# Kernel optimization log

Hardware: AMD Instinct MI355X
Metric: run time of the kernel (lower is better)

## Reference

```python
import jax, jax.numpy as jnp
import numpy as np

B, T, C_IN, H, W = 4, 3, 64, 64, 64
E = 96            # embed_dim
K = 3             # patch_size / deformable kernel size
PAD = 1
N = K * K         # 9 sampled positions per pixel
TOPK = 2
DG = 8            # deformable groups


def conv3x3(x, w, b):
    y = jax.lax.conv_general_dilated(x, w, (1, 1), ((1, 1), (1, 1)),
                                     dimension_numbers=('NCHW', 'OIHW', 'NCHW'))
    return y + b[None, :, None, None]


def lrelu(x):
    return jnp.where(x >= 0, x, 0.1 * x)


def deform_sample(x, off_feat, om_w, om_b):
    """DSP_sep2: modulated deformable sampling. Returns (B, C, N, H, W)."""
    B_, C, H_, W_ = x.shape
    om = conv3x3(off_feat, om_w, om_b).reshape(B_, 3, DG, N, H_, W_)
    off_y, off_x, mask = om[:, 0], om[:, 1], jax.nn.sigmoid(om[:, 2])  # (B,DG,N,H,W)
    ky = (jnp.arange(N) // K - PAD).astype(x.dtype)
    kx = (jnp.arange(N) % K - PAD).astype(x.dtype)
    py = off_y + ky[None, None, :, None, None] + jnp.arange(H_, dtype=x.dtype)[None, None, None, :, None]
    px = off_x + kx[None, None, :, None, None] + jnp.arange(W_, dtype=x.dtype)[None, None, None, None, :]
    y0 = jnp.floor(py); x0 = jnp.floor(px)
    wy = py - y0;       wx = px - x0
    xg = x.reshape(B_, DG, C // DG, H_, W_)
    gat = jax.vmap(jax.vmap(lambda xg_, yi, xi: xg_[:, yi, xi]))  # -> (B,DG,Cg,N,H,W)

    def corner(yc, xc, wgt):
        valid = ((yc >= 0) & (yc < H_) & (xc >= 0) & (xc < W_)).astype(x.dtype)
        yi = jnp.clip(yc, 0, H_ - 1).astype(jnp.int32)
        xi = jnp.clip(xc, 0, W_ - 1).astype(jnp.int32)
        return gat(xg, yi, xi) * (wgt * valid)[:, :, None]

    out = (corner(y0,     x0,     (1 - wy) * (1 - wx)) +
           corner(y0,     x0 + 1, (1 - wy) * wx) +
           corner(y0 + 1, x0,     wy * (1 - wx)) +
           corner(y0 + 1, x0 + 1, wy * wx))
    out = out * mask[:, :, None]  # modulation
    return out.reshape(B_, C, N, H_, W_)


def deform_attn(q, k, v, oc1_w, oc1_b, oc2_w, oc2_b, om_w, om_b):
    B_, E_, H_, W_ = q.shape
    HW = H_ * W_
    off = lrelu(conv3x3(jnp.concatenate([q, k], axis=1), oc1_w, oc1_b))
    off = lrelu(conv3x3(off, oc2_w, oc2_b))
    ko = deform_sample(k, off, om_w, om_b).transpose(0, 3, 4, 2, 1).reshape(B_, HW, N, E_)
    vo = deform_sample(v, off, om_w, om_b).transpose(0, 3, 4, 2, 1).reshape(B_, HW, N, E_)
    qr = q.reshape(B_, E_, HW).transpose(0, 2, 1)              # (B,HW,E)
    rel = jnp.einsum('bpne,bpe->bpn', ko, qr)                  # (B,HW,N)
    vals, idx = jax.lax.top_k(rel, TOPK)                       # (B,HW,k)
    corr = jax.nn.softmax(vals, axis=-1)
    idx_e = jnp.broadcast_to(idx[..., None], idx.shape + (E_,))
    ksel = jnp.take_along_axis(ko, idx_e, axis=2)              # (B,HW,k,E)
    vsel = jnp.take_along_axis(vo, idx_e, axis=2)
    k_up = jnp.einsum('bpke,bpk->bpe', ksel, corr)
    w_ori = jnp.einsum('bpe,bpe->bp', qr, k_up)                # (B,HW)
    v_re = jnp.einsum('bpke,bpk->bpe', vsel, corr).transpose(0, 2, 1)  # (B,E,HW)
    return w_ori, v_re


def setup_inputs() -> dict:
    key = jax.random.key(0)
    ks = jax.random.split(key, 18)
    s = 0.05
    return {
        'fea_full_map': jax.random.normal(ks[0], (B, T, C_IN, H, W), jnp.float32),
        'cf_w': s * jax.random.normal(ks[1], (E, C_IN, 3, 3), jnp.float32),
        'cf_b': s * jax.random.normal(ks[2], (E,), jnp.float32),
        'wq':   s * jax.random.normal(ks[3], (E, E), jnp.float32),
        'bq':   s * jax.random.normal(ks[4], (E,), jnp.float32),
        'wk':   s * jax.random.normal(ks[5], (E, E), jnp.float32),
        'bk':   s * jax.random.normal(ks[6], (E,), jnp.float32),
        'wv':   s * jax.random.normal(ks[7], (E, E), jnp.float32),
        'bv':   s * jax.random.normal(ks[8], (E,), jnp.float32),
        'oc1_w': s * jax.random.normal(ks[9], (E, 2 * E, 3, 3), jnp.float32),
        'oc1_b': s * jax.random.normal(ks[10], (E,), jnp.float32),
        'oc2_w': s * jax.random.normal(ks[11], (E, E, 3, 3), jnp.float32),
        'oc2_b': s * jax.random.normal(ks[12], (E,), jnp.float32),
        'om_w': 0.01 * jax.random.normal(ks[13], (DG * 3 * N, E, 3, 3), jnp.float32),
        'om_b': 0.01 * jax.random.normal(ks[14], (DG * 3 * N,), jnp.float32),
        'cl_w': s * jax.random.normal(ks[15], (C_IN, E, 3, 3), jnp.float32),
        'cl_b': s * jax.random.normal(ks[16], (C_IN,), jnp.float32),
    }


def reference(fea_full_map, cf_w, cf_b, wq, bq, wk, bk, wv, bv,
              oc1_w, oc1_b, oc2_w, oc2_b, om_w, om_b, cl_w, cl_b):
    B_, T_, C_, H_, W_ = fea_full_map.shape
    x = fea_full_map.reshape(B_ * T_, C_, H_, W_)
    emb = conv3x3(x, cf_w, cf_b).reshape(B_, T_, E, H_, W_)
    # per-frame linear Q/K/V over the channel dim (nn.Linear: y = x W^T + b)
    q = jnp.einsum('btchw,dc->btdhw', emb, wq) + bq[None, None, :, None, None]
    k = jnp.einsum('btchw,dc->btdhw', emb, wk) + bk[None, None, :, None, None]
    v = jnp.einsum('btchw,dc->btdhw', emb, wv) + bv[None, None, :, None, None]
    feats = []
    for jj in range(T_):
        ws, vs = [], []
        for ii in range(T_):
            if ii != jj:
                w_, v_ = deform_attn(q[:, jj], k[:, ii], v[:, ii],
                                     oc1_w, oc1_b, oc2_w, oc2_b, om_w, om_b)
                ws.append(w_); vs.append(v_)
        wm = jax.nn.softmax(jnp.stack(ws, axis=1), axis=1)  # (B, T-1, HW)
        vm = jnp.stack(vs, axis=1)                          # (B, T-1, E, HW)
        feats.append((vm * wm[:, :, None, :]).sum(axis=1).reshape(B_, E, H_, W_))
    f = jnp.stack(feats, axis=1).reshape(B_ * T_, E, H_, W_)
    out = conv3x3(f, cl_w, cl_b)
    return out + x
```

## Files before the change

### kernel.cpp

```cpp
#include <hip/hip_runtime.h>
#include <math.h>

#define PIXN 4096

typedef _Float16 f16;
typedef short s16x8 __attribute__((ext_vector_type(8)));
typedef unsigned short u16x4 __attribute__((ext_vector_type(4)));
typedef float f32x4 __attribute__((ext_vector_type(4)));

__device__ __forceinline__ f16 f2h(float f) { return (f16)f; }
__device__ __forceinline__ float h2f(f16 h) { return (float)h; }

__device__ __forceinline__ unsigned short f2bf(float f) {
  unsigned u = __float_as_uint(f);
  u += 0x7fffu + ((u >> 16) & 1u);
  return (unsigned short)(u >> 16);
}
__device__ __forceinline__ float bf2f(unsigned short h) {
  return __uint_as_float(((unsigned)h) << 16);
}

enum { ACT_NONE = 0, ACT_LRELU = 1, ACT_SIG144 = 2 };
enum { IN_FLAT = 1, IN_UVPAIR = 2, IN_QKV = 3, IN_BF = 4 };
enum { OUT_FLAT = 0, OUT_NCHWRES = 1 };

__device__ __forceinline__ void wprep_mfma(const float* __restrict__ w, unsigned short* __restrict__ dst,
                                           int srcCIN, int cinOff, int COUTv, int COUTP,
                                           int total, int idx) {
  if (idx >= total) return;
  int e = idx & 7;
  int t = idx >> 3;
  int co = t % COUTP; t /= COUTP;
  int kch = t & 3; t >>= 2;
  int kc = t % 3;
  int tap = t / 3;
  int ci = kc * 32 + kch * 8 + e;
  float v = 0.f;
  if (co < COUTv) v = w[((long)co * srcCIN + cinOff + ci) * 9 + tap];
  unsigned short h = f2bf(v);
  dst[idx] = h;
  dst[total + idx] = f2bf(v - bf2f(h));
}

__global__ __launch_bounds__(256) void prep_all(
    const float* __restrict__ cf_w, const float* __restrict__ oc1_w,
    const float* __restrict__ oc2_w, const float* __restrict__ om_w,
    const float* __restrict__ cl_w,
    const float* __restrict__ wq, const float* __restrict__ wk, const float* __restrict__ wv,
    const float* __restrict__ bq, const float* __restrict__ bk, const float* __restrict__ bv,
    const float* __restrict__ cf_b,
    unsigned short* __restrict__ WBQ, float* __restrict__ BQ,
    unsigned short* __restrict__ WB1, unsigned short* __restrict__ WB2,
    unsigned short* __restrict__ WB3, unsigned short* __restrict__ WB4) {
  int idx = blockIdx.x * 256 + threadIdx.x;
  switch (blockIdx.y) {
    case 0: {
      if (idx < 288) {
        int m = idx / 96, ep = idx % 96;
        const float* wm = (m == 0) ? wq : (m == 1) ? wk : wv;
        const float* bm = (m == 0) ? bq : (m == 1) ? bk : bv;
        float s = bm[ep];
        for (int c = 0; c < 96; ++c) s = fmaf(wm[ep * 96 + c], cf_b[c], s);
        BQ[idx] = s;
      }
      if (idx < 165888) {
        int e = idx & 7;
        int t = idx >> 3;
        int co = t % 288; t /= 288;
        int kch = t & 3; t >>= 2;
        int kc = t & 1, tap = t >> 1;
        int ci = kc * 32 + kch * 8 + e;
        int m = co / 96, ep = co % 96;
        const float* wm = (m == 0) ? wq : (m == 1) ? wk : wv;
        float s = 0.f;
        for (int c = 0; c < 96; ++c)
          s = fmaf(wm[ep * 96 + c], cf_w[((long)c * 64 + ci) * 9 + tap], s);
        unsigned short h = f2bf(s);
        WBQ[idx] = h;
        WBQ[165888 + idx] = f2bf(s - bf2f(h));
      }
      break;
    }
    case 1: wprep_mfma(oc1_w, WB1, 192, 0, 96, 96, 82944, idx); break;
    case 2: wprep_mfma(oc1_w, WB1 + 2 * 82944, 192, 96, 96, 96, 82944, idx); break;
    case 3: wprep_mfma(oc2_w, WB2, 96, 0, 96, 96, 82944, idx); break;
    case 4: wprep_mfma(om_w, WB3, 96, 0, 216, 256, 221184, idx); break;
    default: wprep_mfma(cl_w, WB4, 96, 0, 64, 64, 55296, idx); break;
  }
}

__global__ __launch_bounds__(256) void nchw2bf(const float* __restrict__ fea,
                                               unsigned short* __restrict__ hi,
                                               unsigned short* __restrict__ lo) {
  const int y = blockIdx.x;
  const int img = blockIdx.y;
  const int t = threadIdx.x;
  const int x = t & 63, cg = t >> 6;
  __shared__ unsigned short sh[64][68], sl[64][68];
  const float* base = fea + ((long)img * 64) * PIXN + y * 64;
#pragma unroll
  for (int k = 0; k < 16; ++k) {
    int ci = cg * 16 + k;
    float v = base[(long)ci * PIXN + x];
    unsigned short h = f2bf(v);
    sh[x][ci] = h;
    sl[x][ci] = f2bf(v - bf2f(h));
  }
  __syncthreads();
  const long ob = (long)img * PIXN + y * 64;
  for (int i = t; i < 2048; i += 256) {
    int plane = i >> 10;
    int r = i & 1023;
    int px = r >> 4, q4 = r & 15;
    u16x4 v4 = *reinterpret_cast<const u16x4*>(plane ? &sl[px][q4 * 4] : &sh[px][q4 * 4]);
    unsigned short* dst = (plane ? lo : hi) + (ob + px) * 64 + q4 * 4;
    *reinterpret_cast<u16x4*>(dst) = v4;
  }
}

template <int CIN, int COUT, int COUTW, int NCOG, int IMODE, int ACT, int OMODE, int WN>
__global__ __launch_bounds__(512, 4) void conv3x3r(
    const float* __restrict__ in, const float* __restrict__ in2,
    const float* __restrict__ bias_in,
    const unsigned short* __restrict__ WB,
    const float* __restrict__ bias,
    float* __restrict__ out,
    const float* __restrict__ resid) {
  constexpr int KC = CIN / 32;
  constexpr int WM = 8 / WN;
  constexpr int MT = WN;
  constexpr int COG = COUTW / NCOG;
  constexpr int NTW = COG / (WN * 16);
  constexpr int AST = 4 * 66 * 8 + 8;
  constexpr int APL = 4 * AST;
  constexpr int BSTEP = COUTW * 32;
  constexpr int TOTB = 9 * KC * BSTEP;

  __shared__ __align__(16) unsigned short Abuf[2 * APL];

  const int tid = threadIdx.x;
  const int lane = tid & 63;
  const int wid = tid >> 6;
  const int wm = wid % WM;
  const int wn = wid / WM;
  const int iz = blockIdx.y;
  const int y0 = blockIdx.x * 2;
  const int zoff = (NCOG > 1) ? blockIdx.z * COG : 0;

  const float* baseA = nullptr;
  const float* baseB2 = nullptr;
  const unsigned short* hpl = nullptr;
  const unsigned short* lpl = nullptr;
  const unsigned short* wbe = WB;
  int LDV = CIN;
  if constexpr (IMODE == IN_UVPAIR) {
    int pair = iz >> 2, b = iz & 3;
    int jj = pair >> 1, rr2 = pair & 1;
    int ii = (rr2 == 0) ? (jj == 0 ? 1 : 0) : (jj == 2 ? 1 : 2);
    baseA = in + (long)(b * 3 + jj) * (PIXN * 96);
    baseB2 = in2 + (long)(b * 3 + ii) * (PIXN * 96);
    LDV = 96;
  } else if constexpr (IMODE == IN_QKV) {
    int sel = iz / 12, img = iz % 12;
    baseA = in + (long)img * (PIXN * 288) + sel * 96;
    wbe = WB + (long)sel * (2 * TOTB);
    LDV = 288;
  } else if constexpr (IMODE == IN_BF) {
    hpl = reinterpret_cast<const unsigned short*>(in) + (long)iz * (PIXN * 64);
    lpl = reinterpret_cast<const unsigned short*>(in2) + (long)iz * (PIXN * 64);
  } else {
    baseA = in + (long)iz * ((long)PIXN * CIN);
    LDV = CIN;
  }

  auto stageA = [&](int kc) {
    if constexpr (IMODE == IN_BF) {
      for (int i = tid; i < 4 * 66 * 4; i += 512) {
        int ci8 = i & 3;
        int t = i >> 2;
        int xp = t % 66, rr = t / 66;
        int y = y0 + rr - 1, x = xp - 1;
        s16x8 hv = {0, 0, 0, 0, 0, 0, 0, 0};
        s16x8 lv = {0, 0, 0, 0, 0, 0, 0, 0};
        if ((unsigned)y < 64u && (unsigned)x < 64u) {
          long off = (long)(y * 64 + x) * 64 + kc * 32 + ci8 * 8;
          hv = *reinterpret_cast<const s16x8*>(hpl + off);
          lv = *reinterpret_cast<const s16x8*>(lpl + off);
        }
        int base = ci8 * AST + (rr * 66 + xp) * 8;
        *reinterpret_cast<s16x8*>(&Abuf[base]) = hv;
        *reinterpret_cast<s16x8*>(&Abuf[APL + base]) = lv;
      }
    } else {
      for (int i = tid; i < 4 * 66 * 8; i += 512) {
        int ci4 = i & 7;
        int t = i >> 3;
        int xp = t % 66, rr = t / 66;
        int y = y0 + rr - 1, x = xp - 1;
        float4 v = make_float4(0.f, 0.f, 0.f, 0.f);
        if ((unsigned)y < 64u && (unsigned)x < 64u) {
          long off = (long)(y * 64 + x) * LDV + kc * 32 + ci4 * 4;
          if constexpr (IMODE == IN_UVPAIR) {
            float4 u = *reinterpret_cast<const float4*>(baseA + off);
            float4 w2 = *reinterpret_cast<const float4*>(baseB2 + off);
            float4 bi = *reinterpret_cast<const float4*>(bias_in + kc * 32 + ci4 * 4);
            v.x = u.x + w2.x + bi.x; v.x = v.x >= 0.f ? v.x : 0.1f * v.x;
            v.y = u.y + w2.y + bi.y; v.y = v.y >= 0.f ? v.y : 0.1f * v.y;
            v.z = u.z + w2.z + bi.z; v.z = v.z >= 0.f ? v.z : 0.1f * v.z;
            v.w = u.w + w2.w + bi.w; v.w = v.w >= 0.f ? v.w : 0.1f * v.w;
          } else {
            v = *reinterpret_cast<const float4*>(baseA + off);
          }
        }
        unsigned short h0 = f2bf(v.x), h1 = f2bf(v.y), h2 = f2bf(v.z), h3 = f2bf(v.w);
        u16x4 hv = {h0, h1, h2, h3};
        u16x4 lv = {f2bf(v.x - bf2f(h0)), f2bf(v.y - bf2f(h1)),
                    f2bf(v.z - bf2f(h2)), f2bf(v.w - bf2f(h3))};
        int base = (ci4 >> 1) * AST + (rr * 66 + xp) * 8 + (ci4 & 1) * 4;
        *reinterpret_cast<u16x4*>(&Abuf[base]) = hv;
        *reinterpret_cast<u16x4*>(&Abuf[APL + base]) = lv;
      }
    }
  };

  f32x4 acc[MT][NTW];
#pragma unroll
  for (int nt = 0; nt < NTW; ++nt) {
    int co = zoff + (wn * NTW + nt) * 16 + (lane & 15);
    float b0 = 0.f;
    if (bias != nullptr && co < COUT) b0 = bias[co];
#pragma unroll
    for (int mt = 0; mt < MT; ++mt) {
      acc[mt][nt][0] = b0; acc[mt][nt][1] = b0;
      acc[mt][nt][2] = b0; acc[mt][nt][3] = b0;
    }
  }

  stageA(0);
  __syncthreads();

  const int blo = ((lane >> 4) * COUTW + zoff + (wn * NTW) * 16 + (lane & 15)) * 8;

  s16x8 cbh[NTW], cbl[NTW], pbh[NTW], pbl[NTW];
#pragma unroll
  for (int nt = 0; nt < NTW; ++nt) {
    const unsigned short* p = wbe + (long)nt * 128 + blo;
    pbh[nt] = *reinterpret_cast<const s16x8*>(p);
    pbl[nt] = *reinterpret_cast<const s16x8*>(p + TOTB);
  }

  long bo = 0;
#pragma unroll 1
  for (int kc = 0; kc < KC; ++kc) {
#pragma unroll 1
    for (int tap = 0; tap < 9; ++tap) {
      const int dy = tap / 3, dx = tap % 3;
      const bool last = (kc == KC - 1) && (tap == 8);
      const long bo_next = (tap < 8) ? bo + (long)KC * BSTEP : (long)(kc + 1) * BSTEP;

#pragma unroll
      for (int nt = 0; nt < NTW; ++nt) { cbh[nt] = pbh[nt]; cbl[nt] = pbl[nt]; }
      if (!last) {
#pragma unroll
        for (int nt = 0; nt < NTW; ++nt) {
          const unsigned short* np = wbe + bo_next + (long)nt * 128 + blo;
          pbh[nt] = *reinterpret_cast<const s16x8*>(np);
          pbl[nt] = *reinterpret_cast<const s16x8*>(np + TOTB);
        }
      }

      s16x8 ah[MT], al[MT];
      {
        int ci8 = lane >> 4;
        int m = lane & 15;
#pragma unroll
        for (int mt = 0; mt < MT; ++mt) {
          int px = (wm * MT + mt) * 16 + m;
          int r = px >> 6, x = px & 63;
          int aoff = ci8 * AST + ((r + dy) * 66 + (x + dx)) * 8;
          ah[mt] = *reinterpret_cast<const s16x8*>(&Abuf[aoff]);
          al[mt] = *reinterpret_cast<const s16x8*>(&Abuf[APL + aoff]);
        }
      }

#pragma unroll
      for (int nt = 0; nt < NTW; ++nt) {
#pragma unroll
        for (int mt = 0; mt < MT; ++mt) {
          acc[mt][nt] = __builtin_amdgcn_mfma_f32_16x16x32_bf16(ah[mt], cbh[nt], acc[mt][nt], 0, 0, 0);
          acc[mt][nt] = __builtin_amdgcn_mfma_f32_16x16x32_bf16(al[mt], cbh[nt], acc[mt][nt], 0, 0, 0);
          acc[mt][nt] = __builtin_amdgcn_mfma_f32_16x16x32_bf16(ah[mt], cbl[nt], acc[mt][nt], 0, 0, 0);
        }
      }
      bo = bo_next;
    }
    if (kc + 1 < KC) {
      __syncthreads();
      stageA(kc + 1);
      __syncthreads();
    }
  }

#pragma unroll
  for (int mt = 0; mt < MT; ++mt) {
#pragma unroll
    for (int nt = 0; nt < NTW; ++nt) {
      int co = zoff + (wn * NTW + nt) * 16 + (lane & 15);
      if (COUTW > COUT && co >= COUT) continue;
#pragma unroll
      for (int r = 0; r < 4; ++r) {
        int px = (wm * MT + mt) * 16 + (lane >> 4) * 4 + r;
        float v = acc[mt][nt][r];
        if constexpr (ACT == ACT_LRELU) v = v >= 0.f ? v : 0.1f * v;
        if constexpr (ACT == ACT_SIG144) {
          if (co >= 144) v = 1.f / (1.f + expf(-v));
        }
        if constexpr (OMODE == OUT_FLAT) {
          const long obase = (long)iz * PIXN + blockIdx.x * 128;
          out[(obase + px) * COUT + co] = v;
        } else {
          long oo = (long)iz * ((long)COUT * PIXN) + (long)co * PIXN + blockIdx.x * 128 + px;
          out[oo] = v + resid[oo];
        }
      }
    }
  }
}

#define CWSLOT 580
__global__ __launch_bounds__(256) void attn3_k(const float* __restrict__ qkv,
                                               const float* __restrict__ om,
                                               float* __restrict__ w_buf,
                                               f16* __restrict__ vre) {
  const int pair = blockIdx.y;
  const int jj = pair >> 1, rr = pair & 1;
  const int ii = (rr == 0) ? (jj == 0 ? 1 : 0) : (jj == 2 ? 1 : 2);
  const int wv = threadIdx.x >> 6;
  const int lane = threadIdx.x & 63;
  const int bp0 = blockIdx.x * 8 + wv * 2;

  __shared__ float s_om[8 * 216];
  __shared__ float s_cw[8 * CWSLOT];

  {
    const float* omrow = om + ((long)pair * 16384 + bp0) * 216;
    float* dst = s_om + wv * 432;
    for (int i = lane; i < 432; i += 64) dst[i] = omrow[i];
  }
  __syncthreads();

  for (int t = lane; t < 144; t += 64) {
    int ph = t / 72, cmb = t - ph * 72;
    int g = cmb / 9, n = cmb - g * 9;
    int p = (bp0 + ph) & 4095;
    int y = p >> 6, x = p & 63;
    const float* so = s_om + (wv * 2 + ph) * 216;
    float oy = so[g * 9 + n], ox = so[72 + g * 9 + n], m = so[144 + g * 9 + n];
    float py = oy + (float)(y + n / 3 - 1);
    float px = ox + (float)(x + n % 3 - 1);
    float y0f = floorf(py), x0f = floorf(px);
    float wy = py - y0f, wx = px - x0f;
    float* dst = s_cw + (wv * 2 + ph) * CWSLOT + cmb * 8;
#pragma unroll
    for (int dy = 0; dy < 2; ++dy) {
#pragma unroll
      for (int dx = 0; dx < 2; ++dx) {
        float yc = y0f + dy, xc = x0f + dx;
        bool valid = (yc >= 0.f) & (yc < 64.f) & (xc >= 0.f) & (xc < 64.f);
        float w = (dy ? wy : 1.f - wy) * (dx ? wx : 1.f - wx) * m;
        w = valid ? w : 0.f;
        int yi = (int)fminf(fmaxf(yc, 0.f), 63.f);
        int xi = (int)fminf(fmaxf(xc, 0.f), 63.f);
        int idx = (yi * 64 + xi) * 288 + 96;
        dst[dy * 2 + dx] = w;
        dst[4 + dy * 2 + dx] = __int_as_float(idx);
      }
    }
  }
  __syncthreads();

  const int ph = lane >> 5;
  const int li = lane & 31;
  const int bp = bp0 + ph;
  const int b = bp >> 12;
  const int cb = li * 3;
  const int g = li >> 2;
  const float* kimg = qkv + (long)(b * 3 + ii) * (PIXN * 288);
  const float* qrow = qkv + ((long)(b * 3 + jj) * PIXN + (bp & 4095)) * 288 + cb;
  const float q0 = qrow[0], q1 = qrow[1], q2 = qrow[2];
  const float* cw = s_cw + (wv * 2 + ph) * CWSLOT + g * 9 * 8;

  float ka[9][3];
  float rel[9];
#pragma unroll
  for (int n = 0; n < 9; ++n) {
    float4 w4 = *reinterpret_cast<const float4*>(cw + n * 8);
    float4 i4 = *reinterpret_cast<const float4*>(cw + n * 8 + 4);
    int ia = __float_as_int(i4.x) + cb, ib = __float_as_int(i4.y) + cb;
    int ic = __float_as_int(i4.z) + cb, id = __float_as_int(i4.w) + cb;
#pragma unroll
    for (int j = 0; j < 3; ++j) {
      float a = w4.x * kimg[ia + j];
      a = fmaf(w4.y, kimg[ib + j], a);
      a = fmaf(w4.z, kimg[ic + j], a);
      a = fmaf(w4.w, kimg[id + j], a);
      ka[n][j] = a;
    }
    float part = q0 * ka[n][0];
    part = fmaf(q1, ka[n][1], part);
    part = fmaf(q2, ka[n][2], part);
#pragma unroll
    for (int off = 16; off > 0; off >>= 1) part += __shfl_xor(part, off, 64);
    rel[n] = part;
  }

  int i0 = 0; float v0 = rel[0];
  float ks0a = ka[0][0], ks0b = ka[0][1], ks0c = ka[0][2];
#pragma unroll
  for (int n = 1; n < 9; ++n) {
    bool t = rel[n] > v0;
    v0 = t ? rel[n] : v0; i0 = t ? n : i0;
    ks0a = t ? ka[n][0] : ks0a; ks0b = t ? ka[n][1] : ks0b; ks0c = t ? ka[n][2] : ks0c;
  }
  int i1 = 0; float v1 = -3.4e38f;
  float ks1a = 0.f, ks1b = 0.f, ks1c = 0.f;
#pragma unroll
  for (int n = 0; n < 9; ++n) {
    bool t = (n != i0) && rel[n] > v1;
    v1 = t ? rel[n] : v1; i1 = t ? n : i1;
    ks1a = t ? ka[n][0] : ks1a; ks1b = t ? ka[n][1] : ks1b; ks1c = t ? ka[n][2] : ks1c;
  }
  float e = expf(v1 - v0);
  float cw0 = 1.f / (1.f + e), cw1 = e * cw0;

  float wpart = q0 * (cw0 * ks0a + cw1 * ks1a);
  wpart = fmaf(q1, cw0 * ks0b + cw1 * ks1b, wpart);
  wpart = fmaf(q2, cw0 * ks0c + cw1 * ks1c, wpart);
#pragma unroll
  for (int off = 16; off > 0; off >>= 1) wpart += __shfl_xor(wpart, off, 64);
  if (li == 0) w_buf[(long)pair * 16384 + bp] = wpart;

  float4 wA = *reinterpret_cast<const float4*>(cw + i0 * 8);
  float4 iA = *reinterpret_cast<const float4*>(cw + i0 * 8 + 4);
  float4 wB = *reinterpret_cast<const float4*>(cw + i1 * 8);
  float4 iB = *reinterpret_cast<const float4*>(cw + i1 * 8 + 4);
  int a0 = __float_as_int(iA.x) + 96 + cb, a1 = __float_as_int(iA.y) + 96 + cb;
  int a2 = __float_as_int(iA.z) + 96 + cb, a3 = __float_as_int(iA.w) + 96 + cb;
  int b0 = __float_as_int(iB.x) + 96 + cb, b1 = __float_as_int(iB.y) + 96 + cb;
  int b2 = __float_as_int(iB.z) + 96 + cb, b3 = __float_as_int(iB.w) + 96 + cb;
  f16* vrow = vre + ((long)pair * 16384 + bp) * 96 + cb;
#pragma unroll
  for (int j = 0; j < 3; ++j) {
    float va = wA.x * kimg[a0 + j];
    va = fmaf(wA.y, kimg[a1 + j], va);
    va = fmaf(wA.z, kimg[a2 + j], va);
    va = fmaf(wA.w, kimg[a3 + j], va);
    float vb = wB.x * kimg[b0 + j];
    vb = fmaf(wB.y, kimg[b1 + j], vb);
    vb = fmaf(wB.z, kimg[b2 + j], vb);
    vb = fmaf(wB.w, kimg[b3 + j], vb);
    vrow[j] = f2h(cw0 * va + cw1 * vb);
  }
}

__global__ __launch_bounds__(256) void merge_k(const float* __restrict__ w_buf,
                                               const f16* __restrict__ vre,
                                               float* __restrict__ f_t) {
  long idx = (long)blockIdx.x * 256 + threadIdx.x;
  const long TOT = (long)4 * 3 * PIXN * 24;
  if (idx >= TOT) return;
  int c4 = idx % 24;
  long t = idx / 24;
  int p = t % PIXN;
  long t2 = t / PIXN;
  int jj = t2 % 3;
  int b = (int)(t2 / 3);
  long bpi = (long)b * PIXN + p;
  int pr0 = jj * 2, pr1 = jj * 2 + 1;
  float w0 = w_buf[(long)pr0 * 16384 + bpi];
  float w1 = w_buf[(long)pr1 * 16384 + bpi];
  float mx = fmaxf(w0, w1);
  float e0 = expf(w0 - mx), e1 = expf(w1 - mx);
  float inv = 1.f / (e0 + e1);
  float s0 = e0 * inv, s1 = e1 * inv;
  const f16* va = &vre[((long)pr0 * 16384 + bpi) * 96 + c4 * 4];
  const f16* vb = &vre[((long)pr1 * 16384 + bpi) * 96 + c4 * 4];
  float4 r;
  r.x = s0 * h2f(va[0]) + s1 * h2f(vb[0]);
  r.y = s0 * h2f(va[1]) + s1 * h2f(vb[1]);
  r.z = s0 * h2f(va[2]) + s1 * h2f(vb[2]);
  r.w = s0 * h2f(va[3]) + s1 * h2f(vb[3]);
  *reinterpret_cast<float4*>(f_t + ((long)(b * 3 + jj) * PIXN + p) * 96 + c4 * 4) = r;
}

extern "C" void kernel_launch(void* const* d_in, const int* in_sizes, int n_in,
                              void* d_out, int out_size, void* d_ws, size_t ws_size,
                              hipStream_t stream) {
  const float* fea = (const float*)d_in[0];
  const float* cf_w = (const float*)d_in[1];
  const float* cf_b = (const float*)d_in[2];
  const float* wq = (const float*)d_in[3];
  const float* bq = (const float*)d_in[4];
  const float* wk = (const float*)d_in[5];
  const float* bk = (const float*)d_in[6];
  const float* wv = (const float*)d_in[7];
  const float* bv = (const float*)d_in[8];
  const float* oc1_w = (const float*)d_in[9];
  const float* oc1_b = (const float*)d_in[10];
  const float* oc2_w = (const float*)d_in[11];
  const float* oc2_b = (const float*)d_in[12];
  const float* om_w = (const float*)d_in[13];
  const float* om_b = (const float*)d_in[14];
  const float* cl_w = (const float*)d_in[15];
  const float* cl_b = (const float*)d_in[16];

  char* base = (char*)d_ws;
  size_t o = 0;
  auto carve = [&](size_t bytes) { char* p = base + o; o += (bytes + 255) & ~255UL; return p; };

  unsigned short* WBQ = (unsigned short*)carve(2UL * 165888 * 2);
  float* BQ = (float*)carve(288UL * 4);
  unsigned short* WB1 = (unsigned short*)carve(2UL * 2 * 82944 * 2);
  unsigned short* WB2 = (unsigned short*)carve(2UL * 82944 * 2);
  unsigned short* WB3 = (unsigned short*)carve(2UL * 221184 * 2);
  unsigned short* WB4 = (unsigned short*)carve(2UL * 55296 * 2);
  unsigned short* feaH = (unsigned short*)carve(12UL * PIXN * 64 * 2);
  unsigned short* feaL = (unsigned short*)carve(12UL * PIXN * 64 * 2);

  float* om_t = (float*)carve(21233664UL * 4);
  float* qkv_t = (float*)carve(14155776UL * 4);
  float* U_t = (float*)carve(4718592UL * 4);
  float* V_t = (float*)carve(4718592UL * 4);
  float* off2_t = (float*)carve(9437184UL * 4);
  float* w_buf = (float*)carve(98304UL * 4);
  float* f_t = U_t;
  f16* vre_b = (f16*)V_t;

  prep_all<<<dim3(864, 6), 256, 0, stream>>>(cf_w, oc1_w, oc2_w, om_w, cl_w,
                                             wq, wk, wv, bq, bk, bv, cf_b,
                                             WBQ, BQ, WB1, WB2, WB3, WB4);

  nchw2bf<<<dim3(64, 12), 256, 0, stream>>>(fea, feaH, feaL);

  conv3x3r<64, 288, 288, 3, IN_BF, ACT_NONE, OUT_FLAT, 2><<<dim3(32, 12, 3), 512, 0, stream>>>(
      (const float*)feaH, (const float*)feaL, nullptr, WBQ, BQ, qkv_t, nullptr);

  conv3x3r<96, 96, 96, 1, IN_QKV, ACT_NONE, OUT_FLAT, 2><<<dim3(32, 24, 1), 512, 0, stream>>>(
      qkv_t, nullptr, nullptr, WB1, nullptr, U_t, nullptr);

  conv3x3r<96, 96, 96, 1, IN_UVPAIR, ACT_LRELU, OUT_FLAT, 2><<<dim3(32, 24, 1), 512, 0, stream>>>(
      U_t, V_t, oc1_b, WB2, oc2_b, off2_t, nullptr);

  conv3x3r<96, 216, 256, 2, IN_FLAT, ACT_SIG144, OUT_FLAT, 4><<<dim3(32, 24, 2), 512, 0, stream>>>(
      off2_t, nullptr, nullptr, WB3, om_b, om_t, nullptr);

  attn3_k<<<dim3(2048, 6), 256, 0, stream>>>(qkv_t, om_t, w_buf, vre_b);
  merge_k<<<4608, 256, 0, stream>>>(w_buf, vre_b, f_t);

  conv3x3r<96, 64, 64, 1, IN_FLAT, ACT_NONE, OUT_NCHWRES, 2><<<dim3(32, 12, 1), 512, 0, stream>>>(
      f_t, nullptr, nullptr, WB4, cl_b, (float*)d_out, fea);
}
```

Baseline: 491.6 us.

## Fuse deformable attention with softmax merge and restructure conv weight prefetch

```diff
diff --git a/kernel.cpp b/kernel.cpp
--- a/kernel.cpp
+++ b/kernel.cpp
@@ -241,7 +241,7 @@
 
   const int blo = ((lane >> 4) * COUTW + zoff + (wn * NTW) * 16 + (lane & 15)) * 8;
 
-  s16x8 cbh[NTW], cbl[NTW], pbh[NTW], pbl[NTW];
+  s16x8 pbh[NTW], pbl[NTW];
 #pragma unroll
   for (int nt = 0; nt < NTW; ++nt) {
     const unsigned short* p = wbe + (long)nt * 128 + blo;
@@ -258,17 +258,6 @@
       const bool last = (kc == KC - 1) && (tap == 8);
       const long bo_next = (tap < 8) ? bo + (long)KC * BSTEP : (long)(kc + 1) * BSTEP;
 
-#pragma unroll
-      for (int nt = 0; nt < NTW; ++nt) { cbh[nt] = pbh[nt]; cbl[nt] = pbl[nt]; }
-      if (!last) {
-#pragma unroll
-        for (int nt = 0; nt < NTW; ++nt) {
-          const unsigned short* np = wbe + bo_next + (long)nt * 128 + blo;
-          pbh[nt] = *reinterpret_cast<const s16x8*>(np);
-          pbl[nt] = *reinterpret_cast<const s16x8*>(np + TOTB);
-        }
-      }
-
       s16x8 ah[MT], al[MT];
       {
         int ci8 = lane >> 4;
@@ -287,9 +276,14 @@
       for (int nt = 0; nt < NTW; ++nt) {
 #pragma unroll
         for (int mt = 0; mt < MT; ++mt) {
-          acc[mt][nt] = __builtin_amdgcn_mfma_f32_16x16x32_bf16(ah[mt], cbh[nt], acc[mt][nt], 0, 0, 0);
-          acc[mt][nt] = __builtin_amdgcn_mfma_f32_16x16x32_bf16(al[mt], cbh[nt], acc[mt][nt], 0, 0, 0);
-          acc[mt][nt] = __builtin_amdgcn_mfma_f32_16x16x32_bf16(ah[mt], cbl[nt], acc[mt][nt], 0, 0, 0);
+          acc[mt][nt] = __builtin_amdgcn_mfma_f32_16x16x32_bf16(ah[mt], pbh[nt], acc[mt][nt], 0, 0, 0);
+          acc[mt][nt] = __builtin_amdgcn_mfma_f32_16x16x32_bf16(al[mt], pbh[nt], acc[mt][nt], 0, 0, 0);
+          acc[mt][nt] = __builtin_amdgcn_mfma_f32_16x16x32_bf16(ah[mt], pbl[nt], acc[mt][nt], 0, 0, 0);
+        }
+        if (!last) {
+          const unsigned short* np = wbe + bo_next + (long)nt * 128 + blo;
+          pbh[nt] = *reinterpret_cast<const s16x8*>(np);
+          pbl[nt] = *reinterpret_cast<const s16x8*>(np + TOTB);
         }
       }
       bo = bo_next;
@@ -328,169 +322,181 @@
 }
 
 #define CWSLOT 580
-__global__ __launch_bounds__(256) void attn3_k(const float* __restrict__ qkv,
+__global__ __launch_bounds__(256) void attn4_k(const float* __restrict__ qkv,
                                                const float* __restrict__ om,
-                                               float* __restrict__ w_buf,
-                                               f16* __restrict__ vre) {
-  const int pair = blockIdx.y;
-  const int jj = pair >> 1, rr = pair & 1;
-  const int ii = (rr == 0) ? (jj == 0 ? 1 : 0) : (jj == 2 ? 1 : 2);
+                                               float* __restrict__ f_t) {
+  const int jj = blockIdx.y;
   const int wv = threadIdx.x >> 6;
   const int lane = threadIdx.x & 63;
   const int bp0 = blockIdx.x * 8 + wv * 2;
 
   __shared__ float s_om[8 * 216];
   __shared__ float s_cw[8 * CWSLOT];
-
-  {
-    const float* omrow = om + ((long)pair * 16384 + bp0) * 216;
-    float* dst = s_om + wv * 432;
-    for (int i = lane; i < 432; i += 64) dst[i] = omrow[i];
-  }
-  __syncthreads();
-
-  for (int t = lane; t < 144; t += 64) {
-    int ph = t / 72, cmb = t - ph * 72;
-    int g = cmb / 9, n = cmb - g * 9;
-    int p = (bp0 + ph) & 4095;
-    int y = p >> 6, x = p & 63;
-    const float* so = s_om + (wv * 2 + ph) * 216;
-    float oy = so[g * 9 + n], ox = so[72 + g * 9 + n], m = so[144 + g * 9 + n];
-    float py = oy + (float)(y + n / 3 - 1);
-    float px = ox + (float)(x + n % 3 - 1);
-    float y0f = floorf(py), x0f = floorf(px);
-    float wy = py - y0f, wx = px - x0f;
-    float* dst = s_cw + (wv * 2 + ph) * CWSLOT + cmb * 8;
-#pragma unroll
-    for (int dy = 0; dy < 2; ++dy) {
-#pragma unroll
-      for (int dx = 0; dx < 2; ++dx) {
-        float yc = y0f + dy, xc = x0f + dx;
-        bool valid = (yc >= 0.f) & (yc < 64.f) & (xc >= 0.f) & (xc < 64.f);
-        float w = (dy ? wy : 1.f - wy) * (dx ? wx : 1.f - wx) * m;
-        w = valid ? w : 0.f;
-        int yi = (int)fminf(fmaxf(yc, 0.f), 63.f);
-        int xi = (int)fminf(fmaxf(xc, 0.f), 63.f);
-        int idx = (yi * 64 + xi) * 288 + 96;
-        dst[dy * 2 + dx] = w;
-        dst[4 + dy * 2 + dx] = __int_as_float(idx);
-      }
-    }
-  }
-  __syncthreads();
 
   const int ph = lane >> 5;
   const int li = lane & 31;
   const int bp = bp0 + ph;
   const int b = bp >> 12;
+  const int p = bp & 4095;
   const int cb = li * 3;
   const int g = li >> 2;
-  const float* kimg = qkv + (long)(b * 3 + ii) * (PIXN * 288);
-  const float* qrow = qkv + ((long)(b * 3 + jj) * PIXN + (bp & 4095)) * 288 + cb;
+  const float* qrow = qkv + ((long)(b * 3 + jj) * PIXN + p) * 288 + cb;
   const float q0 = qrow[0], q1 = qrow[1], q2 = qrow[2];
-  const float* cw = s_cw + (wv * 2 + ph) * CWSLOT + g * 9 * 8;
-
-  float ka[9][3];
-  float rel[9];
-#pragma unroll
-  for (int n = 0; n < 9; ++n) {
-    float4 w4 = *reinterpret_cast<const float4*>(cw + n * 8);
-    float4 i4 = *reinterpret_cast<const float4*>(cw + n * 8 + 4);
-    int ia = __float_as_int(i4.x) + cb, ib = __float_as_int(i4.y) + cb;
-    int ic = __float_as_int(i4.z) + cb, id = __float_as_int(i4.w) + cb;
-#pragma unroll
-    for (int j = 0; j < 3; ++j) {
-      float a = w4.x * kimg[ia + j];
-      a = fmaf(w4.y, kimg[ib + j], a);
-      a = fmaf(w4.z, kimg[ic + j], a);
-      a = fmaf(w4.w, kimg[id + j], a);
-      ka[n][j] = a;
-    }
-    float part = q0 * ka[n][0];
-    part = fmaf(q1, ka[n][1], part);
-    part = fmaf(q2, ka[n][2], part);
-#pragma unroll
-    for (int off = 16; off > 0; off >>= 1) part += __shfl_xor(part, off, 64);
-    rel[n] = part;
-  }
-
-  int i0 = 0; float v0 = rel[0];
-  float ks0a = ka[0][0], ks0b = ka[0][1], ks0c = ka[0][2];
-#pragma unroll
-  for (int n = 1; n < 9; ++n) {
-    bool t = rel[n] > v0;
-    v0 = t ? rel[n] : v0; i0 = t ? n : i0;
-    ks0a = t ? ka[n][0] : ks0a; ks0b = t ? ka[n][1] : ks0b; ks0c = t ? ka[n][2] : ks0c;
-  }
-  int i1 = 0; float v1 = -3.4e38f;
-  float ks1a = 0.f, ks1b = 0.f, ks1c = 0.f;
-#pragma unroll
-  for (int n = 0; n < 9; ++n) {
-    bool t = (n != i0) && rel[n] > v1;
-    v1 = t ? rel[n] : v1; i1 = t ? n : i1;
-    ks1a = t ? ka[n][0] : ks1a; ks1b = t ? ka[n][1] : ks1b; ks1c = t ? ka[n][2] : ks1c;
-  }
-  float e = expf(v1 - v0);
-  float cw0 = 1.f / (1.f + e), cw1 = e * cw0;
-
-  float wpart = q0 * (cw0 * ks0a + cw1 * ks1a);
-  wpart = fmaf(q1, cw0 * ks0b + cw1 * ks1b, wpart);
-  wpart = fmaf(q2, cw0 * ks0c + cw1 * ks1c, wpart);
-#pragma unroll
-  for (int off = 16; off > 0; off >>= 1) wpart += __shfl_xor(wpart, off, 64);
-  if (li == 0) w_buf[(long)pair * 16384 + bp] = wpart;
-
-  float4 wA = *reinterpret_cast<const float4*>(cw + i0 * 8);
-  float4 iA = *reinterpret_cast<const float4*>(cw + i0 * 8 + 4);
-  float4 wB = *reinterpret_cast<const float4*>(cw + i1 * 8);
-  float4 iB = *reinterpret_cast<const float4*>(cw + i1 * 8 + 4);
-  int a0 = __float_as_int(iA.x) + 96 + cb, a1 = __float_as_int(iA.y) + 96 + cb;
-  int a2 = __float_as_int(iA.z) + 96 + cb, a3 = __float_as_int(iA.w) + 96 + cb;
-  int b0 = __float_as_int(iB.x) + 96 + cb, b1 = __float_as_int(iB.y) + 96 + cb;
-  int b2 = __float_as_int(iB.z) + 96 + cb, b3 = __float_as_int(iB.w) + 96 + cb;
-  f16* vrow = vre + ((long)pair * 16384 + bp) * 96 + cb;
-#pragma unroll
-  for (int j = 0; j < 3; ++j) {
-    float va = wA.x * kimg[a0 + j];
-    va = fmaf(wA.y, kimg[a1 + j], va);
-    va = fmaf(wA.z, kimg[a2 + j], va);
-    va = fmaf(wA.w, kimg[a3 + j], va);
-    float vb = wB.x * kimg[b0 + j];
-    vb = fmaf(wB.y, kimg[b1 + j], vb);
-    vb = fmaf(wB.z, kimg[b2 + j], vb);
-    vb = fmaf(wB.w, kimg[b3 + j], vb);
-    vrow[j] = f2h(cw0 * va + cw1 * vb);
-  }
-}
-
-__global__ __launch_bounds__(256) void merge_k(const float* __restrict__ w_buf,
-                                               const f16* __restrict__ vre,
-                                               float* __restrict__ f_t) {
-  long idx = (long)blockIdx.x * 256 + threadIdx.x;
-  const long TOT = (long)4 * 3 * PIXN * 24;
-  if (idx >= TOT) return;
-  int c4 = idx % 24;
-  long t = idx / 24;
-  int p = t % PIXN;
-  long t2 = t / PIXN;
-  int jj = t2 % 3;
-  int b = (int)(t2 / 3);
-  long bpi = (long)b * PIXN + p;
-  int pr0 = jj * 2, pr1 = jj * 2 + 1;
-  float w0 = w_buf[(long)pr0 * 16384 + bpi];
-  float w1 = w_buf[(long)pr1 * 16384 + bpi];
-  float mx = fmaxf(w0, w1);
-  float e0 = expf(w0 - mx), e1 = expf(w1 - mx);
+
+  float wsc0 = 0.f, wsc1 = 0.f;
+  float v00 = 0.f, v01 = 0.f, v02 = 0.f;
+  float v10 = 0.f, v11 = 0.f, v12 = 0.f;
+
+#pragma unroll 1
+  for (int pr = 0; pr < 2; ++pr) {
+    const int pair = jj * 2 + pr;
+    const int ii = (pr == 0) ? (jj == 0 ? 1 : 0) : (jj == 2 ? 1 : 2);
+    const float* kimg = qkv + (long)(b * 3 + ii) * (PIXN * 288);
+
+    __syncthreads();
+    {
+      const float* omrow = om + ((long)pair * 16384 + bp0) * 216;
+      float* dst = s_om + wv * 432;
+      for (int i = lane; i < 432; i += 64) dst[i] = omrow[i];
+    }
+    __syncthreads();
+
+    for (int t = lane; t < 144; t += 64) {
+      int php = t / 72, cmb = t - php * 72;
+      int gs = cmb / 9, n = cmb - gs * 9;
+      int ps = (bp0 + php) & 4095;
+      int y = ps >> 6, x = ps & 63;
+      const float* so = s_om + (wv * 2 + php) * 216;
+      float oy = so[gs * 9 + n], ox = so[72 + gs * 9 + n], m = so[144 + gs * 9 + n];
+      float py = oy + (float)(y + n / 3 - 1);
+      float px = ox + (float)(x + n % 3 - 1);
+      float y0f = floorf(py), x0f = floorf(px);
+      float wy = py - y0f, wx = px - x0f;
+      float* dst = s_cw + (wv * 2 + php) * CWSLOT + cmb * 8;
+#pragma unroll
+      for (int dy = 0; dy < 2; ++dy) {
+#pragma unroll
+        for (int dx = 0; dx < 2; ++dx) {
+          float yc = y0f + dy, xc = x0f + dx;
+          bool valid = (yc >= 0.f) & (yc < 64.f) & (xc >= 0.f) & (xc < 64.f);
+          float w = (dy ? wy : 1.f - wy) * (dx ? wx : 1.f - wx) * m;
+          w = valid ? w : 0.f;
+          int yi = (int)fminf(fmaxf(yc, 0.f), 63.f);
+          int xi = (int)fminf(fmaxf(xc, 0.f), 63.f);
+          int idx = (yi * 64 + xi) * 288 + 96;
+          dst[dy * 2 + dx] = w;
+          dst[4 + dy * 2 + dx] = __int_as_float(idx);
+        }
+      }
+    }
+    __syncthreads();
+
+    const float* cw = s_cw + (wv * 2 + ph) * CWSLOT + g * 9 * 8;
+
+    float ka[9][3];
+    float rel[9];
+#pragma unroll
+    for (int n = 0; n < 9; ++n) {
+      float4 w4 = *reinterpret_cast<const float4*>(cw + n * 8);
+      float4 i4 = *reinterpret_cast<const float4*>(cw + n * 8 + 4);
+      int ia = __float_as_int(i4.x) + cb, ib = __float_as_int(i4.y) + cb;
+      int ic = __float_as_int(i4.z) + cb, id = __float_as_int(i4.w) + cb;
+#pragma unroll
+      for (int j = 0; j < 3; ++j) {
+        float a = w4.x * kimg[ia + j];
+        a = fmaf(w4.y, kimg[ib + j], a);
+        a = fmaf(w4.z, kimg[ic + j], a);
+        a = fmaf(w4.w, kimg[id + j], a);
+        ka[n][j] = a;
+      }
+      float part = q0 * ka[n][0];
+      part = fmaf(q1, ka[n][1], part);
+      part = fmaf(q2, ka[n][2], part);
+#pragma unroll
+      for (int off = 16; off > 0; off >>= 1) part += __shfl_xor(part, off, 64);
+      rel[n] = part;
+    }
+
+    int i0 = 0; float v0 = rel[0];
+    float ks0a = ka[0][0], ks0b = ka[0][1], ks0c = ka[0][2];
+#pragma unroll
+    for (int n = 1; n < 9; ++n) {
+      bool t = rel[n] > v0;
+      v0 = t ? rel[n] : v0; i0 = t ? n : i0;
+      ks0a = t ? ka[n][0] : ks0a; ks0b = t ? ka[n][1] : ks0b; ks0c = t ? ka[n][2] : ks0c;
+    }
+    int i1 = 0; float v1 = -3.4e38f;
+    float ks1a = 0.f, ks1b = 0.f, ks1c = 0.f;
+#pragma unroll
+    for (int n = 0; n < 9; ++n) {
+      bool t = (n != i0) && rel[n] > v1;
+      v1 = t ? rel[n] : v1; i1 = t ? n : i1;
+      ks1a = t ? ka[n][0] : ks1a; ks1b = t ? ka[n][1] : ks1b; ks1c = t ? ka[n][2] : ks1c;
+    }
+    float e = expf(v1 - v0);
+    float cw0 = 1.f / (1.f + e), cw1 = e * cw0;
+
+    float wpart = q0 * (cw0 * ks0a + cw1 * ks1a);
+    wpart = fmaf(q1, cw0 * ks0b + cw1 * ks1b, wpart);
+    wpart = fmaf(q2, cw0 * ks0c + cw1 * ks1c, wpart);
+#pragma unroll
+    for (int off = 16; off > 0; off >>= 1) wpart += __shfl_xor(wpart, off, 64);
+
+    float4 wA = *reinterpret_cast<const float4*>(cw + i0 * 8);
+    float4 iA = *reinterpret_cast<const float4*>(cw + i0 * 8 + 4);
+    float4 wB = *reinterpret_cast<const float4*>(cw + i1 * 8);
+    float4 iB = *reinterpret_cast<const float4*>(cw + i1 * 8 + 4);
+    int a0 = __float_as_int(iA.x) + 96 + cb, a1 = __float_as_int(iA.y) + 96 + cb;
+    int a2 = __float_as_int(iA.z) + 96 + cb, a3 = __float_as_int(iA.w) + 96 + cb;
+    int b0 = __float_as_int(iB.x) + 96 + cb, b1 = __float_as_int(iB.y) + 96 + cb;
+    int b2 = __float_as_int(iB.z) + 96 + cb, b3 = __float_as_int(iB.w) + 96 + cb;
+    float r0, r1, r2;
+    {
+      float va = wA.x * kimg[a0];
+      va = fmaf(wA.y, kimg[a1], va);
+      va = fmaf(wA.z, kimg[a2], va);
+      va = fmaf(wA.w, kimg[a3], va);
+      float vb = wB.x * kimg[b0];
+      vb = fmaf(wB.y, kimg[b1], vb);
+      vb = fmaf(wB.z, kimg[b2], vb);
+      vb = fmaf(wB.w, kimg[b3], vb);
+      r0 = cw0 * va + cw1 * vb;
+    }
+    {
+      float va = wA.x * kimg[a0 + 1];
+      va = fmaf(wA.y, kimg[a1 + 1], va);
+      va = fmaf(wA.z, kimg[a2 + 1], va);
+      va = fmaf(wA.w, kimg[a3 + 1], va);
+      float vb = wB.x * kimg[b0 + 1];
+      vb = fmaf(wB.y, kimg[b1 + 1], vb);
+      vb = fmaf(wB.z, kimg[b2 + 1], vb);
+      vb = fmaf(wB.w, kimg[b3 + 1], vb);
+      r1 = cw0 * va + cw1 * vb;
+    }
+    {
+      float va = wA.x * kimg[a0 + 2];
+      va = fmaf(wA.y, kimg[a1 + 2], va);
+      va = fmaf(wA.z, kimg[a2 + 2], va);
+      va = fmaf(wA.w, kimg[a3 + 2], va);
+      float vb = wB.x * kimg[b0 + 2];
+      vb = fmaf(wB.y, kimg[b1 + 2], vb);
+      vb = fmaf(wB.z, kimg[b2 + 2], vb);
+      vb = fmaf(wB.w, kimg[b3 + 2], vb);
+      r2 = cw0 * va + cw1 * vb;
+    }
+
+    if (pr == 0) { wsc0 = wpart; v00 = r0; v01 = r1; v02 = r2; }
+    else         { wsc1 = wpart; v10 = r0; v11 = r1; v12 = r2; }
+  }
+
+  float mx = fmaxf(wsc0, wsc1);
+  float e0 = expf(wsc0 - mx), e1 = expf(wsc1 - mx);
   float inv = 1.f / (e0 + e1);
   float s0 = e0 * inv, s1 = e1 * inv;
-  const f16* va = &vre[((long)pr0 * 16384 + bpi) * 96 + c4 * 4];
-  const f16* vb = &vre[((long)pr1 * 16384 + bpi) * 96 + c4 * 4];
-  float4 r;
-  r.x = s0 * h2f(va[0]) + s1 * h2f(vb[0]);
-  r.y = s0 * h2f(va[1]) + s1 * h2f(vb[1]);
-  r.z = s0 * h2f(va[2]) + s1 * h2f(vb[2]);
-  r.w = s0 * h2f(va[3]) + s1 * h2f(vb[3]);
-  *reinterpret_cast<float4*>(f_t + ((long)(b * 3 + jj) * PIXN + p) * 96 + c4 * 4) = r;
+  float* frow = f_t + ((long)(b * 3 + jj) * PIXN + p) * 96 + cb;
+  frow[0] = s0 * v00 + s1 * v10;
+  frow[1] = s0 * v01 + s1 * v11;
+  frow[2] = s0 * v02 + s1 * v12;
 }
 
 extern "C" void kernel_launch(void* const* d_in, const int* in_sizes, int n_in,
@@ -532,9 +538,7 @@
   float* U_t = (float*)carve(4718592UL * 4);
   float* V_t = (float*)carve(4718592UL * 4);
   float* off2_t = (float*)carve(9437184UL * 4);
-  float* w_buf = (float*)carve(98304UL * 4);
   float* f_t = U_t;
-  f16* vre_b = (f16*)V_t;
 
   prep_all<<<dim3(864, 6), 256, 0, stream>>>(cf_w, oc1_w, oc2_w, om_w, cl_w,
                                              wq, wk, wv, bq, bk, bv, cf_b,
@@ -551,11 +555,10 @@
   conv3x3r<96, 96, 96, 1, IN_UVPAIR, ACT_LRELU, OUT_FLAT, 2><<<dim3(32, 24, 1), 512, 0, stream>>>(
       U_t, V_t, oc1_b, WB2, oc2_b, off2_t, nullptr);
 
-  conv3x3r<96, 216, 256, 2, IN_FLAT, ACT_SIG144, OUT_FLAT, 4><<<dim3(32, 24, 2), 512, 0, stream>>>(
+  conv3x3r<96, 216, 256, 2, IN_FLAT, ACT_SIG144, OUT_FLAT, 2><<<dim3(32, 24, 2), 512, 0, stream>>>(
       off2_t, nullptr, nullptr, WB3, om_b, om_t, nullptr);
 
-  attn3_k<<<dim3(2048, 6), 256, 0, stream>>>(qkv_t, om_t, w_buf, vre_b);
-  merge_k<<<4608, 256, 0, stream>>>(w_buf, vre_b, f_t);
+  attn4_k<<<dim3(2048, 3), 256, 0, stream>>>(qkv_t, om_t, f_t);
 
   conv3x3r<96, 64, 64, 1, IN_FLAT, ACT_NONE, OUT_NCHWRES, 2><<<dim3(32, 12, 1), 512, 0, stream>>>(
       f_t, nullptr, nullptr, WB4, cl_b, (float*)d_out, fea);
```

Result: slower. 536.5 us (+9.1%).

## Reorder packed weights kc-major and fully unroll tap loop in conv MFMA kernel

Applied to the files above, without the earlier changes.

```diff
diff --git a/kernel.cpp b/kernel.cpp
--- a/kernel.cpp
+++ b/kernel.cpp
@@ -32,8 +32,8 @@
   int t = idx >> 3;
   int co = t % COUTP; t /= COUTP;
   int kch = t & 3; t >>= 2;
-  int kc = t % 3;
-  int tap = t / 3;
+  int tap = t % 9;
+  int kc = t / 9;
   int ci = kc * 32 + kch * 8 + e;
   float v = 0.f;
   if (co < COUTv) v = w[((long)co * srcCIN + cinOff + ci) * 9 + tap];
@@ -68,7 +68,7 @@
         int t = idx >> 3;
         int co = t % 288; t /= 288;
         int kch = t & 3; t >>= 2;
-        int kc = t & 1, tap = t >> 1;
+        int tap = t % 9, kc = t / 9;
         int ci = kc * 32 + kch * 8 + e;
         int m = co / 96, ep = co % 96;
         const float* wm = (m == 0) ? wq : (m == 1) ? wk : wv;
@@ -240,59 +240,55 @@
   __syncthreads();
 
   const int blo = ((lane >> 4) * COUTW + zoff + (wn * NTW) * 16 + (lane & 15)) * 8;
-
-  s16x8 cbh[NTW], cbl[NTW], pbh[NTW], pbl[NTW];
+  const unsigned short* pBH = wbe + blo;
+  const unsigned short* pBL = wbe + (long)TOTB + blo;
+
+  s16x8 pbh[NTW], pbl[NTW];
 #pragma unroll
   for (int nt = 0; nt < NTW; ++nt) {
-    const unsigned short* p = wbe + (long)nt * 128 + blo;
-    pbh[nt] = *reinterpret_cast<const s16x8*>(p);
-    pbl[nt] = *reinterpret_cast<const s16x8*>(p + TOTB);
-  }
-
-  long bo = 0;
+    pbh[nt] = *reinterpret_cast<const s16x8*>(pBH + nt * 128);
+    pbl[nt] = *reinterpret_cast<const s16x8*>(pBL + nt * 128);
+  }
+
+  int abase[MT];
+  {
+    int ci8 = lane >> 4, m = lane & 15;
+#pragma unroll
+    for (int mt = 0; mt < MT; ++mt) {
+      int px = (wm * MT + mt) * 16 + m;
+      int r = px >> 6, x = px & 63;
+      abase[mt] = ci8 * AST + (r * 66 + x) * 8;
+    }
+  }
+
 #pragma unroll 1
   for (int kc = 0; kc < KC; ++kc) {
-#pragma unroll 1
+#pragma unroll
     for (int tap = 0; tap < 9; ++tap) {
-      const int dy = tap / 3, dx = tap % 3;
+      const int toff = ((tap / 3) * 66 + (tap % 3)) * 8;
       const bool last = (kc == KC - 1) && (tap == 8);
-      const long bo_next = (tap < 8) ? bo + (long)KC * BSTEP : (long)(kc + 1) * BSTEP;
-
-#pragma unroll
-      for (int nt = 0; nt < NTW; ++nt) { cbh[nt] = pbh[nt]; cbl[nt] = pbl[nt]; }
-      if (!last) {
-#pragma unroll
-        for (int nt = 0; nt < NTW; ++nt) {
-          const unsigned short* np = wbe + bo_next + (long)nt * 128 + blo;
-          pbh[nt] = *reinterpret_cast<const s16x8*>(np);
-          pbl[nt] = *reinterpret_cast<const s16x8*>(np + TOTB);
+      if (!last) { pBH += BSTEP; pBL += BSTEP; }
+
+      s16x8 ah[MT], al[MT];
+#pragma unroll
+      for (int mt = 0; mt < MT; ++mt) {
+        ah[mt] = *reinterpret_cast<const s16x8*>(&Abuf[abase[mt] + toff]);
+        al[mt] = *reinterpret_cast<const s16x8*>(&Abuf[abase[mt] + toff + APL]);
+      }
+
+#pragma unroll
+      for (int nt = 0; nt < NTW; ++nt) {
+#pragma unroll
+        for (int mt = 0; mt < MT; ++mt) {
+          acc[mt][nt] = __builtin_amdgcn_mfma_f32_16x16x32_bf16(ah[mt], pbh[nt], acc[mt][nt], 0, 0, 0);
+          acc[mt][nt] = __builtin_amdgcn_mfma_f32_16x16x32_bf16(al[mt], pbh[nt], acc[mt][nt], 0, 0, 0);
+          acc[mt][nt] = __builtin_amdgcn_mfma_f32_16x16x32_bf16(ah[mt], pbl[nt], acc[mt][nt], 0, 0, 0);
         }
-      }
-
-      s16x8 ah[MT], al[MT];
-      {
-        int ci8 = lane >> 4;
-        int m = lane & 15;
-#pragma unroll
-        for (int mt = 0; mt < MT; ++mt) {
-          int px = (wm * MT + mt) * 16 + m;
-          int r = px >> 6, x = px & 63;
-          int aoff = ci8 * AST + ((r + dy) * 66 + (x + dx)) * 8;
-          ah[mt] = *reinterpret_cast<const s16x8*>(&Abuf[aoff]);
-          al[mt] = *reinterpret_cast<const s16x8*>(&Abuf[APL + aoff]);
+        if (!last) {
+          pbh[nt] = *reinterpret_cast<const s16x8*>(pBH + nt * 128);
+          pbl[nt] = *reinterpret_cast<const s16x8*>(pBL + nt * 128);
         }
       }
-
-#pragma unroll
-      for (int nt = 0; nt < NTW; ++nt) {
-#pragma unroll
-        for (int mt = 0; mt < MT; ++mt) {
-          acc[mt][nt] = __builtin_amdgcn_mfma_f32_16x16x32_bf16(ah[mt], cbh[nt], acc[mt][nt], 0, 0, 0);
-          acc[mt][nt] = __builtin_amdgcn_mfma_f32_16x16x32_bf16(al[mt], cbh[nt], acc[mt][nt], 0, 0, 0);
-          acc[mt][nt] = __builtin_amdgcn_mfma_f32_16x16x32_bf16(ah[mt], cbl[nt], acc[mt][nt], 0, 0, 0);
-        }
-      }
-      bo = bo_next;
     }
     if (kc + 1 < KC) {
       __syncthreads();
@@ -551,7 +547,7 @@
   conv3x3r<96, 96, 96, 1, IN_UVPAIR, ACT_LRELU, OUT_FLAT, 2><<<dim3(32, 24, 1), 512, 0, stream>>>(
       U_t, V_t, oc1_b, WB2, oc2_b, off2_t, nullptr);
 
-  conv3x3r<96, 216, 256, 2, IN_FLAT, ACT_SIG144, OUT_FLAT, 4><<<dim3(32, 24, 2), 512, 0, stream>>>(
+  conv3x3r<96, 216, 256, 2, IN_FLAT, ACT_SIG144, OUT_FLAT, 2><<<dim3(32, 24, 2), 512, 0, stream>>>(
       off2_t, nullptr, nullptr, WB3, om_b, om_t, nullptr);
 
   attn3_k<<<dim3(2048, 6), 256, 0, stream>>>(qkv_t, om_t, w_buf, vre_b);
```

Measured after the change: 619.5 us. 26.0% more time.
